# Kernel tuning notes

Measured on AMD Instinct MI355X. Metric: run time of the kernel, lower is better.

The kernel has to match this reference:

```python
import jax, jax.numpy as jnp
import numpy as np
import math

HEADS = 16
D = 1024
HEAD_DIM = D // HEADS
SEQ = 2048
BATCH = 4
LN_EPS = 1e-5


def setup_inputs() -> dict:
    key = jax.random.key(0)
    ks = jax.random.split(key, 7)
    s = 1.0 / math.sqrt(HEAD_DIM)
    return {
        "q": jax.random.normal(ks[0], (SEQ, BATCH, D), dtype=jnp.float32),
        "k": jax.random.normal(ks[1], (SEQ, BATCH, D), dtype=jnp.float32),
        "v": jax.random.normal(ks[2], (SEQ, BATCH, D), dtype=jnp.float32),
        "Wq": jax.random.normal(ks[3], (HEAD_DIM, HEAD_DIM), dtype=jnp.float32) * s,
        "Wk": jax.random.normal(ks[4], (HEAD_DIM, HEAD_DIM), dtype=jnp.float32) * s,
        "Wv": jax.random.normal(ks[5], (HEAD_DIM, HEAD_DIM), dtype=jnp.float32) * s,
        "Wl": jax.random.normal(ks[6], (D, D), dtype=jnp.float32) * (1.0 / math.sqrt(D)),
        "gamma": jnp.ones((D,), dtype=jnp.float32),
        "beta": jnp.zeros((D,), dtype=jnp.float32),
    }


def reference(q, k, v, Wq, Wk, Wv, Wl, gamma, beta):
    # q, k, v: [seq_len, batch, d]  (seq-first, as in the torch module)
    q_len, batch = q.shape[0], q.shape[1]
    k_len, v_len = k.shape[0], v.shape[0]
    # Faithful to torch: reshape (NOT transpose) seq-first tensor into
    # (batch, len, heads, head_dim), then per-head linear (x @ W.T, no bias).
    Qh = jnp.einsum('bqhd,ed->bqhe', q.reshape(batch, q_len, HEADS, HEAD_DIM), Wq)
    Kh = jnp.einsum('bkhd,ed->bkhe', k.reshape(batch, k_len, HEADS, HEAD_DIM), Wk)
    Vh = jnp.einsum('bvhd,ed->bvhe', v.reshape(batch, v_len, HEADS, HEAD_DIM), Wv)
    # Scores scaled by sqrt(d) (full model dim), as in the original.
    scores = jnp.einsum('bqhd,bkhd->bhqk', Qh, Kh) / math.sqrt(D)
    attn = jax.nn.softmax(scores, axis=-1)  # dropout p=0.0 -> identity
    out = jnp.einsum('bhqk,bkhd->bqhd', attn, Vh)  # [b, q, h, d]
    concat = out.reshape(q_len, batch, D)
    lin = concat @ Wl.T
    mean = jnp.mean(lin, axis=-1, keepdims=True)
    var = jnp.var(lin, axis=-1, keepdims=True)
    ln = (lin - mean) * jax.lax.rsqrt(var + LN_EPS) * gamma + beta
    return q + ln
```

## Files before the change

kernel.cpp:

```cpp
#include <hip/hip_runtime.h>

#define LOG2E 1.4426950408889634f

typedef __attribute__((ext_vector_type(8))) short short8_t;
typedef __attribute__((ext_vector_type(4))) float floatx4;
typedef __attribute__((ext_vector_type(16))) float floatx16;

#define MFMA(a,b,c)   __builtin_amdgcn_mfma_f32_16x16x32_bf16(a,b,c,0,0,0)
#define MFMA32(a,b,c) __builtin_amdgcn_mfma_f32_32x32x16_bf16(a,b,c,0,0,0)
#define GLOAD(g, l) __builtin_amdgcn_global_load_lds( \
    (const __attribute__((address_space(1))) unsigned int*)(g), \
    (__attribute__((address_space(3))) unsigned int*)(l), 16, 0, 0)

__device__ __forceinline__ unsigned short f2bf(float f){
    unsigned u = __float_as_uint(f);
    u = u + 0x7FFFu + ((u >> 16) & 1u);
    return (unsigned short)(u >> 16);
}
__device__ __forceinline__ float bf2f(unsigned short s){
    return __uint_as_float(((unsigned)s) << 16);
}
__device__ __forceinline__ unsigned cvtpk(float lo, float hi){
    unsigned r;
    asm("v_cvt_pk_bf16_f32 %0, %1, %2" : "=v"(r) : "v"(lo), "v"(hi));
    return r;
}
__device__ __forceinline__ void plswap(unsigned &a, unsigned &b){
    asm volatile("v_permlane32_swap_b32 %0, %1" : "+v"(a), "+v"(b));
}

union U8 { unsigned u[4]; short8_t s8; };

__global__ __launch_bounds__(256) void proj_kernel(
    const float* __restrict__ Xq, const float* __restrict__ Xk, const float* __restrict__ Xv,
    const float* __restrict__ Wq, const float* __restrict__ Wk, const float* __restrict__ Wv,
    unsigned short* __restrict__ qp, unsigned short* __restrict__ kp, unsigned short* __restrict__ vp)
{
    const int rt = blockIdx.x;
    const int h  = blockIdx.y;
    const int sel= blockIdx.z;
    const float* X = (sel==0)?Xq:(sel==1)?Xk:Xv;
    const float* W = (sel==0)?Wq:(sel==1)?Wk:Wv;
    unsigned short* O = (sel==0)?qp:(sel==1)?kp:vp;
    const float qs = (sel==0) ? ((1.0f/32.0f)*LOG2E) : 1.0f;

    const int t  = threadIdx.x;
    const int w  = t >> 6, l = t & 63;
    const int r5 = l & 31;
    const int hf = l >> 5;

    const int row0 = rt*128 + w*32;

    short8_t a[4];
    {
        const float* xb = X + (size_t)(row0 + r5)*1024 + h*64 + hf*8;
        #pragma unroll
        for (int kb=0; kb<4; kb++){
            float4 f0 = *reinterpret_cast<const float4*>(xb + kb*16);
            float4 f1 = *reinterpret_cast<const float4*>(xb + kb*16 + 4);
            U8 u;
            u.u[0] = cvtpk(f0.x, f0.y); u.u[1] = cvtpk(f0.z, f0.w);
            u.u[2] = cvtpk(f1.x, f1.y); u.u[3] = cvtpk(f1.z, f1.w);
            a[kb] = u.s8;
        }
    }
    short8_t b[2][4];
    #pragma unroll
    for (int nb=0; nb<2; nb++){
        const float* wb = W + (size_t)(nb*32 + r5)*64 + hf*8;
        #pragma unroll
        for (int kb=0; kb<4; kb++){
            float4 f0 = *reinterpret_cast<const float4*>(wb + kb*16);
            float4 f1 = *reinterpret_cast<const float4*>(wb + kb*16 + 4);
            U8 u;
            u.u[0] = cvtpk(f0.x, f0.y); u.u[1] = cvtpk(f0.z, f0.w);
            u.u[2] = cvtpk(f1.x, f1.y); u.u[3] = cvtpk(f1.z, f1.w);
            b[nb][kb] = u.s8;
        }
    }

    floatx16 acc[2] = {};
    #pragma unroll
    for (int nb=0; nb<2; nb++)
        #pragma unroll
        for (int kb=0; kb<4; kb++)
            acc[nb] = MFMA32(a[kb], b[nb][kb], acc[nb]);

    const int c   = rt >> 4;
    const size_t chbase = (size_t)(c*16 + h);

    #pragma unroll
    for (int nb=0; nb<2; nb++){
        const int e = nb*32 + r5;
        #pragma unroll
        for (int m=0; m<4; m++){
            unsigned p01 = cvtpk(acc[nb][4*m]*qs,   acc[nb][4*m+1]*qs);
            unsigned p23 = cvtpk(acc[nb][4*m+2]*qs, acc[nb][4*m+3]*qs);
            #pragma unroll
            for (int i=0; i<4; i++){
                unsigned short val = (unsigned short)
                    ((i==0)?p01 : (i==1)?(p01>>16) : (i==2)?p23 : (p23>>16));
                const int gr = row0 + i + 8*m + 4*hf;
                const int s  = gr & 2047;
                size_t addr;
                if (sel == 0){
                    addr = (chbase*2048 + s)*64 + e;
                } else {
                    const int kt_ = s >> 6, rl = s & 63;
                    const size_t tbase = (chbase*32 + kt_)*4096;
                    if (sel == 1)
                        addr = tbase + rl*64 + (((e>>3) ^ (rl&7))<<3) + (e&7);
                    else
                        addr = tbase + e*64 + (((rl>>3) ^ (e&7))<<3) + (rl&7);
                }
                O[addr] = val;
            }
        }
    }
}

__global__ __launch_bounds__(256,1) void attn_kernel(
    const unsigned short* __restrict__ qp, const unsigned short* __restrict__ kp,
    const unsigned short* __restrict__ vp, unsigned short* __restrict__ ob)
{
    const int bswz = blockIdx.x;
    const int xr   = bswz & 7;
    const int rest = bswz >> 3;
    const int qt   = rest & 15;
    const int p    = xr + 8*(rest >> 4);
    const int hd   = p & 15;
    const int c    = p >> 4;

    const int t  = threadIdx.x;
    const int w  = t >> 6, l = t & 63;
    const int r5 = l & 31;
    const int hf = l >> 5;

    __shared__ unsigned short Ks[3][64][64];
    __shared__ unsigned short Vs[3][64][64];

    const size_t chq = ((size_t)(c*16 + hd))*2048*64;
    const size_t cht = ((size_t)(c*16 + hd))*32*4096;

    short8_t aq[4];
    {
        const unsigned short* qrow = qp + chq + (size_t)(qt*128 + w*32 + r5)*64 + hf*8;
        #pragma unroll
        for (int kb=0;kb<4;kb++)
            aq[kb] = *reinterpret_cast<const short8_t*>(qrow + kb*16);
    }

    const char* kbase = (const char*)(kp + cht) + w*2048 + l*16;
    const char* vbase = (const char*)(vp + cht) + w*2048 + l*16;
    char* kdst0 = (char*)(&Ks[0][0][0]) + w*2048;
    char* vdst0 = (char*)(&Vs[0][0][0]) + w*2048;

    #define ATTN_STAGE(buf, kt) do { \
        const char* ks_ = kbase + (size_t)(kt)*8192; \
        const char* vs_ = vbase + (size_t)(kt)*8192; \
        char* kd_ = kdst0 + (buf)*8192; \
        char* vd_ = vdst0 + (buf)*8192; \
        GLOAD(ks_,      kd_);      GLOAD(ks_+1024, kd_+1024); \
        GLOAD(vs_,      vd_);      GLOAD(vs_+1024, vd_+1024); \
    } while(0)

    const int x7 = r5 & 7;

    U8 onesu;
    onesu.u[0] = 0x3F803F80u; onesu.u[1] = 0x3F803F80u;
    onesu.u[2] = 0x3F803F80u; onesu.u[3] = 0x3F803F80u;
    const short8_t ones8 = onesu.s8;

    floatx16 oa[2] = {};
    floatx16 lsv = {};
    short8_t Fp[4];

    ATTN_STAGE(0, 0);

    int cur = 0;
    for (int kt=0; kt<32; kt++){
        const int nxt = (cur==2) ? 0 : cur+1;
        const int prv = (cur==0) ? 2 : cur-1;

        asm volatile("s_waitcnt vmcnt(0)" ::: "memory");
        __builtin_amdgcn_s_barrier();
        __builtin_amdgcn_sched_barrier(0);

        if (kt < 31) ATTN_STAGE(nxt, kt+1);

        const unsigned short* Kc = &Ks[cur][0][0];
        const unsigned short* Vp = &Vs[prv][0][0];

        floatx16 sacc[2] = {};
        __builtin_amdgcn_s_setprio(1);
        #pragma unroll
        for (int mb=0;mb<2;mb++){
            #pragma unroll
            for (int kb=0;kb<4;kb++){
                short8_t kf = *reinterpret_cast<const short8_t*>(
                    Kc + (mb*32 + r5)*64 + (((kb*2 + hf) ^ x7)<<3));
                sacc[mb] = MFMA32(kf, aq[kb], sacc[mb]);
            }
        }
        if (kt > 0){
            #pragma unroll
            for (int db=0;db<2;db++){
                #pragma unroll
                for (int kb2=0;kb2<4;kb2++){
                    short8_t vf = *reinterpret_cast<const short8_t*>(
                        Vp + (db*32 + r5)*64 + (((kb2*2 + hf) ^ x7)<<3));
                    oa[db] = MFMA32(vf, Fp[kb2], oa[db]);
                }
            }
            #pragma unroll
            for (int f=0;f<4;f++) lsv = MFMA32(ones8, Fp[f], lsv);
        }
        __builtin_amdgcn_s_setprio(0);

        #pragma unroll
        for (int mb=0;mb<2;mb++)
            #pragma unroll
            for (int i=0;i<16;i++)
                sacc[mb][i] = __builtin_amdgcn_exp2f(sacc[mb][i]);

        #pragma unroll
        for (int mb=0;mb<2;mb++){
            unsigned lo[4], hi[4];
            #pragma unroll
            for (int m=0;m<4;m++){
                lo[m] = cvtpk(sacc[mb][4*m],   sacc[mb][4*m+1]);
                hi[m] = cvtpk(sacc[mb][4*m+2], sacc[mb][4*m+3]);
            }
            #pragma unroll
            for (int hk=0;hk<2;hk++){
                unsigned a = lo[2*hk], b = lo[2*hk+1];
                unsigned cc = hi[2*hk], d = hi[2*hk+1];
                plswap(a, b);
                plswap(cc, d);
                U8 fu;
                fu.u[0] = a; fu.u[1] = cc; fu.u[2] = b; fu.u[3] = d;
                Fp[mb*2 + hk] = fu.s8;
            }
        }

        cur = nxt;
    }

    {
        const int prv = (cur==0) ? 2 : cur-1;
        const unsigned short* Vp = &Vs[prv][0][0];
        #pragma unroll
        for (int db=0;db<2;db++){
            #pragma unroll
            for (int kb2=0;kb2<4;kb2++){
                short8_t vf = *reinterpret_cast<const short8_t*>(
                    Vp + (db*32 + r5)*64 + (((kb2*2 + hf) ^ x7)<<3));
                oa[db] = MFMA32(vf, Fp[kb2], oa[db]);
            }
        }
        #pragma unroll
        for (int f=0;f<4;f++) lsv = MFMA32(ones8, Fp[f], lsv);
    }

    const float inv = 1.0f / lsv[0];
    const size_t grow = (size_t)c*2048 + qt*128 + w*32 + r5;
    unsigned short* obp = ob + grow*1024 + hd*64 + hf*4;
    #pragma unroll
    for (int db=0;db<2;db++){
        #pragma unroll
        for (int m=0;m<4;m++){
            ushort4 u;
            u.x = f2bf(oa[db][4*m]*inv);   u.y = f2bf(oa[db][4*m+1]*inv);
            u.z = f2bf(oa[db][4*m+2]*inv); u.w = f2bf(oa[db][4*m+3]*inv);
            *reinterpret_cast<ushort4*>(obp + db*32 + m*8) = u;
        }
    }
}

__global__ __launch_bounds__(256) void wlconv_kernel(const float* __restrict__ W,
                                                     unsigned short* __restrict__ O)
{
    int i = (blockIdx.x*256 + threadIdx.x)*4;
    float4 f = *reinterpret_cast<const float4*>(W + i);
    ushort4 u;
    u.x = f2bf(f.x); u.y = f2bf(f.y); u.z = f2bf(f.z); u.w = f2bf(f.w);
    *reinterpret_cast<ushort4*>(O + i) = u;
}

__global__ __launch_bounds__(256) void gemm_kernel(
    const unsigned short* __restrict__ A, const unsigned short* __restrict__ B,
    unsigned short* __restrict__ C)
{
    const int bm = blockIdx.x, bn = blockIdx.y;
    __shared__ unsigned short As[2][128][64];
    __shared__ unsigned short Bs[2][128][64];
    const int t = threadIdx.x, w = t>>6, l = t&63;
    const int l15 = l&15, l4 = l>>4;
    const int wm = w>>1, wn = w&1;

    const char* asrc = (const char*)A + ((size_t)(bm*128 + w*32 + (l>>3)))*2048 + (l&7)*16;
    const char* bsrc = (const char*)B + ((size_t)(bn*128 + w*32 + (l>>3)))*2048 + (l&7)*16;
    char* adst = (char*)(&As[0][0][0]) + w*4096;
    char* bdst = (char*)(&Bs[0][0][0]) + w*4096;

    #define GEMM_STAGE(buf, kt) do { \
        const char* as_ = asrc + (size_t)(kt)*128; \
        const char* bs_ = bsrc + (size_t)(kt)*128; \
        char* ad_ = adst + (buf)*16384; \
        char* bd_ = bdst + (buf)*16384; \
        GLOAD(as_,          ad_);        GLOAD(as_+16384,  ad_+1024); \
        GLOAD(as_+32768,    ad_+2048);   GLOAD(as_+49152,  ad_+3072); \
        GLOAD(bs_,          bd_);        GLOAD(bs_+16384,  bd_+1024); \
        GLOAD(bs_+32768,    bd_+2048);   GLOAD(bs_+49152,  bd_+3072); \
    } while(0)

    floatx4 acc[4][4] = {};

    GEMM_STAGE(0, 0);

    for (int kt=0; kt<16; kt++){
        const int cur = kt & 1;
        if (kt < 15){
            GEMM_STAGE(cur^1, kt+1);
            asm volatile("s_waitcnt vmcnt(8)" ::: "memory");
        } else {
            asm volatile("s_waitcnt vmcnt(0)" ::: "memory");
        }
        __builtin_amdgcn_s_barrier();
        __builtin_amdgcn_sched_barrier(0);

        #pragma unroll
        for (int kk=0;kk<2;kk++){
            short8_t a[4], b[4];
            #pragma unroll
            for (int mt=0;mt<4;mt++)
                a[mt] = *reinterpret_cast<const short8_t*>(&As[cur][wm*64 + mt*16 + l15][kk*32 + l4*8]);
            #pragma unroll
            for (int nt=0;nt<4;nt++)
                b[nt] = *reinterpret_cast<const short8_t*>(&Bs[cur][wn*64 + nt*16 + l15][kk*32 + l4*8]);
            __builtin_amdgcn_s_setprio(1);
            #pragma unroll
            for (int mt=0;mt<4;mt++)
                #pragma unroll
                for (int nt=0;nt<4;nt++)
                    acc[mt][nt] = MFMA(a[mt], b[nt], acc[mt][nt]);
            __builtin_amdgcn_s_setprio(0);
        }

        __builtin_amdgcn_sched_barrier(0);
        __builtin_amdgcn_s_barrier();
    }

    #pragma unroll
    for (int mt=0;mt<4;mt++)
        #pragma unroll
        for (int nt=0;nt<4;nt++)
            #pragma unroll
            for (int j=0;j<4;j++){
                int row = bm*128 + wm*64 + mt*16 + l4*4 + j;
                int col = bn*128 + wn*64 + nt*16 + l15;
                C[(size_t)row*1024 + col] = f2bf(acc[mt][nt][j]);
            }
}

__global__ __launch_bounds__(256) void ln_kernel(
    const unsigned short* __restrict__ lin, const float* __restrict__ qin,
    const float* __restrict__ gamma, const float* __restrict__ beta, float* __restrict__ out)
{
    const int r = blockIdx.x, t = threadIdx.x;
    const unsigned short* row = lin + (size_t)r*1024;
    uint2 u = *reinterpret_cast<const uint2*>(row + t*4);
    float v0 = bf2f((unsigned short)(u.x & 0xffffu));
    float v1 = bf2f((unsigned short)(u.x >> 16));
    float v2 = bf2f((unsigned short)(u.y & 0xffffu));
    float v3 = bf2f((unsigned short)(u.y >> 16));
    float s  = v0+v1+v2+v3;
    float sq = v0*v0+v1*v1+v2*v2+v3*v3;
    #pragma unroll
    for (int d=1; d<64; d<<=1){ s += __shfl_xor(s, d); sq += __shfl_xor(sq, d); }
    __shared__ float red[8];
    if ((t&63)==0){ red[(t>>6)*2] = s; red[(t>>6)*2+1] = sq; }
    __syncthreads();
    s  = red[0]+red[2]+red[4]+red[6];
    sq = red[1]+red[3]+red[5]+red[7];
    float mean = s*(1.f/1024.f);
    float var  = sq*(1.f/1024.f) - mean*mean;
    float rs   = rsqrtf(var + 1e-5f);
    int base = r*1024 + t*4;
    float4 qv = *reinterpret_cast<const float4*>(qin + base);
    float4 g  = *reinterpret_cast<const float4*>(gamma + t*4);
    float4 b  = *reinterpret_cast<const float4*>(beta + t*4);
    float4 o;
    o.x = qv.x + (v0-mean)*rs*g.x + b.x;
    o.y = qv.y + (v1-mean)*rs*g.y + b.y;
    o.z = qv.z + (v2-mean)*rs*g.z + b.z;
    o.w = qv.w + (v3-mean)*rs*g.w + b.w;
    *reinterpret_cast<float4*>(out + base) = o;
}

extern "C" void kernel_launch(void* const* d_in, const int* in_sizes, int n_in,
                              void* d_out, int out_size, void* d_ws, size_t ws_size,
                              hipStream_t stream)
{
    (void)in_sizes; (void)n_in; (void)out_size; (void)ws_size;
    const float* q     = (const float*)d_in[0];
    const float* k     = (const float*)d_in[1];
    const float* v     = (const float*)d_in[2];
    const float* Wq    = (const float*)d_in[3];
    const float* Wk    = (const float*)d_in[4];
    const float* Wv    = (const float*)d_in[5];
    const float* Wl    = (const float*)d_in[6];
    const float* gamma = (const float*)d_in[7];
    const float* beta  = (const float*)d_in[8];
    float* out = (float*)d_out;

    char* ws = (char*)d_ws;
    unsigned short* qp  = (unsigned short*)(ws);
    unsigned short* kp  = (unsigned short*)(ws + (16u<<20));
    unsigned short* vp  = (unsigned short*)(ws + (32u<<20));
    unsigned short* ob  = (unsigned short*)(ws + (48u<<20));
    unsigned short* lin = (unsigned short*)(ws);
    unsigned short* wlb = (unsigned short*)(ws + (16u<<20));

    proj_kernel <<<dim3(64,16,3),  256, 0, stream>>>(q,k,v, Wq,Wk,Wv, qp,kp,vp);
    attn_kernel <<<dim3(1024),     256, 0, stream>>>(qp,kp,vp, ob);
    wlconv_kernel<<<dim3(1024),    256, 0, stream>>>(Wl, wlb);
    gemm_kernel <<<dim3(64,8),     256, 0, stream>>>(ob, wlb, lin);
    ln_kernel   <<<dim3(8192),     256, 0, stream>>>(lin, q, gamma, beta, out);
}
```

Measured before the change: 182.9 us.

## Write attention output and Wl in pre-tiled swizzled layout for contiguous GEMM loads

```diff
diff --git a/kernel.cpp b/kernel.cpp
--- a/kernel.cpp
+++ b/kernel.cpp
@@ -30,6 +30,7 @@
 }
 
 union U8 { unsigned u[4]; short8_t s8; };
+
 
 __global__ __launch_bounds__(256) void proj_kernel(
     const float* __restrict__ Xq, const float* __restrict__ Xk, const float* __restrict__ Xv,
@@ -136,7 +137,7 @@
     const int r5 = l & 31;
     const int hf = l >> 5;
 
-    __shared__ unsigned short Ks[3][64][64];
+    __shared__ unsigned short Ks[2][64][64];
     __shared__ unsigned short Vs[3][64][64];
 
     const size_t chq = ((size_t)(c*16 + hd))*2048*64;
@@ -155,11 +156,11 @@
     char* kdst0 = (char*)(&Ks[0][0][0]) + w*2048;
     char* vdst0 = (char*)(&Vs[0][0][0]) + w*2048;
 
-    #define ATTN_STAGE(buf, kt) do { \
+    #define ATTN_STAGE(kbuf, vbuf, kt) do { \
         const char* ks_ = kbase + (size_t)(kt)*8192; \
         const char* vs_ = vbase + (size_t)(kt)*8192; \
-        char* kd_ = kdst0 + (buf)*8192; \
-        char* vd_ = vdst0 + (buf)*8192; \
+        char* kd_ = kdst0 + (kbuf)*8192; \
+        char* vd_ = vdst0 + (vbuf)*8192; \
         GLOAD(ks_,      kd_);      GLOAD(ks_+1024, kd_+1024); \
         GLOAD(vs_,      vd_);      GLOAD(vs_+1024, vd_+1024); \
     } while(0)
@@ -175,21 +176,22 @@
     floatx16 lsv = {};
     short8_t Fp[4];
 
-    ATTN_STAGE(0, 0);
-
-    int cur = 0;
+    ATTN_STAGE(0, 0, 0);
+
+    int vcur = 0;
     for (int kt=0; kt<32; kt++){
-        const int nxt = (cur==2) ? 0 : cur+1;
-        const int prv = (cur==0) ? 2 : cur-1;
+        const int kcur = kt & 1;
+        const int vnxt = (vcur==2) ? 0 : vcur+1;
+        const int vprv = (vcur==0) ? 2 : vcur-1;
 
         asm volatile("s_waitcnt vmcnt(0)" ::: "memory");
         __builtin_amdgcn_s_barrier();
         __builtin_amdgcn_sched_barrier(0);
 
-        if (kt < 31) ATTN_STAGE(nxt, kt+1);
-
-        const unsigned short* Kc = &Ks[cur][0][0];
-        const unsigned short* Vp = &Vs[prv][0][0];
+        if (kt < 31) ATTN_STAGE(kcur^1, vnxt, kt+1);
+
+        const unsigned short* Kc = &Ks[kcur][0][0];
+        const unsigned short* Vp = &Vs[vprv][0][0];
 
         floatx16 sacc[2] = {};
         __builtin_amdgcn_s_setprio(1);
@@ -243,12 +245,12 @@
             }
         }
 
-        cur = nxt;
+        vcur = vnxt;
     }
 
     {
-        const int prv = (cur==0) ? 2 : cur-1;
-        const unsigned short* Vp = &Vs[prv][0][0];
+        const int vprv = (vcur==0) ? 2 : vcur-1;
+        const unsigned short* Vp = &Vs[vprv][0][0];
         #pragma unroll
         for (int db=0;db<2;db++){
             #pragma unroll
@@ -263,8 +265,9 @@
     }
 
     const float inv = 1.0f / lsv[0];
-    const size_t grow = (size_t)c*2048 + qt*128 + w*32 + r5;
-    unsigned short* obp = ob + grow*1024 + hd*64 + hf*4;
+    const int rl_ = w*32 + r5;
+    unsigned short* obimg = ob + ((size_t)((c*16 + qt)*16 + hd))*8192 + rl_*64;
+    const int x7o = rl_ & 7;
     #pragma unroll
     for (int db=0;db<2;db++){
         #pragma unroll
@@ -272,7 +275,7 @@
             ushort4 u;
             u.x = f2bf(oa[db][4*m]*inv);   u.y = f2bf(oa[db][4*m+1]*inv);
             u.z = f2bf(oa[db][4*m+2]*inv); u.w = f2bf(oa[db][4*m+3]*inv);
-            *reinterpret_cast<ushort4*>(obp + db*32 + m*8) = u;
+            *reinterpret_cast<ushort4*>(obimg + (((db*4+m) ^ x7o)<<3) + hf*4) = u;
         }
     }
 }
@@ -281,10 +284,14 @@
                                                      unsigned short* __restrict__ O)
 {
     int i = (blockIdx.x*256 + threadIdx.x)*4;
+    const int n = i >> 10, k = i & 1023;
     float4 f = *reinterpret_cast<const float4*>(W + i);
     ushort4 u;
     u.x = f2bf(f.x); u.y = f2bf(f.y); u.z = f2bf(f.z); u.w = f2bf(f.w);
-    *reinterpret_cast<ushort4*>(O + i) = u;
+    const int rl = n & 127, cl = k & 63;
+    size_t off = ((size_t)((n>>7)*16 + (k>>6)))*8192 + rl*64
+               + (((cl>>3) ^ (rl&7))<<3) + (cl&7);
+    *reinterpret_cast<ushort4*>(O + off) = u;
 }
 
 __global__ __launch_bounds__(256) void gemm_kernel(
@@ -297,21 +304,22 @@
     const int t = threadIdx.x, w = t>>6, l = t&63;
     const int l15 = l&15, l4 = l>>4;
     const int wm = w>>1, wn = w&1;
-
-    const char* asrc = (const char*)A + ((size_t)(bm*128 + w*32 + (l>>3)))*2048 + (l&7)*16;
-    const char* bsrc = (const char*)B + ((size_t)(bn*128 + w*32 + (l>>3)))*2048 + (l&7)*16;
+    const int x7g = l15 & 7;
+
+    const char* abase = (const char*)A + (size_t)bm*16*16384 + w*4096 + l*16;
+    const char* bbase = (const char*)B + (size_t)bn*16*16384 + w*4096 + l*16;
     char* adst = (char*)(&As[0][0][0]) + w*4096;
     char* bdst = (char*)(&Bs[0][0][0]) + w*4096;
 
     #define GEMM_STAGE(buf, kt) do { \
-        const char* as_ = asrc + (size_t)(kt)*128; \
-        const char* bs_ = bsrc + (size_t)(kt)*128; \
+        const char* as_ = abase + (size_t)(kt)*16384; \
+        const char* bs_ = bbase + (size_t)(kt)*16384; \
         char* ad_ = adst + (buf)*16384; \
         char* bd_ = bdst + (buf)*16384; \
-        GLOAD(as_,          ad_);        GLOAD(as_+16384,  ad_+1024); \
-        GLOAD(as_+32768,    ad_+2048);   GLOAD(as_+49152,  ad_+3072); \
-        GLOAD(bs_,          bd_);        GLOAD(bs_+16384,  bd_+1024); \
-        GLOAD(bs_+32768,    bd_+2048);   GLOAD(bs_+49152,  bd_+3072); \
+        GLOAD(as_,       ad_);        GLOAD(as_+1024,  ad_+1024); \
+        GLOAD(as_+2048,  ad_+2048);   GLOAD(as_+3072,  ad_+3072); \
+        GLOAD(bs_,       bd_);        GLOAD(bs_+1024,  bd_+1024); \
+        GLOAD(bs_+2048,  bd_+2048);   GLOAD(bs_+3072,  bd_+3072); \
     } while(0)
 
     floatx4 acc[4][4] = {};
@@ -333,11 +341,17 @@
         for (int kk=0;kk<2;kk++){
             short8_t a[4], b[4];
             #pragma unroll
-            for (int mt=0;mt<4;mt++)
-                a[mt] = *reinterpret_cast<const short8_t*>(&As[cur][wm*64 + mt*16 + l15][kk*32 + l4*8]);
-            #pragma unroll
-            for (int nt=0;nt<4;nt++)
-                b[nt] = *reinterpret_cast<const short8_t*>(&Bs[cur][wn*64 + nt*16 + l15][kk*32 + l4*8]);
+            for (int mt=0;mt<4;mt++){
+                int row = wm*64 + mt*16 + l15;
+                a[mt] = *reinterpret_cast<const short8_t*>(
+                    &As[cur][0][0] + row*64 + (((kk*4 + l4) ^ x7g)<<3));
+            }
+            #pragma unroll
+            for (int nt=0;nt<4;nt++){
+                int row = wn*64 + nt*16 + l15;
+                b[nt] = *reinterpret_cast<const short8_t*>(
+                    &Bs[cur][0][0] + row*64 + (((kk*4 + l4) ^ x7g)<<3));
+            }
             __builtin_amdgcn_s_setprio(1);
             #pragma unroll
             for (int mt=0;mt<4;mt++)
```

New measurement: 175.5 us. -4.0%, faster.
